# Kernel tuning notes

Measured on AMD Instinct MI355X. Metric: run time of the kernel, lower is better.

The kernel has to match this reference:

```python
import jax, jax.numpy as jnp
import numpy as np

N_NODES = 50000
N_EDGES = 1_600_000
IN_CH, HID_CH, NUM_CLS = 256, 128, 64
THRESHOLD = 0.5  # default forward arg


def setup_inputs() -> dict:
    key = jax.random.key(0)
    k1, k2, k3, k4 = jax.random.split(key, 4)
    x = jax.random.normal(k1, (N_NODES, IN_CH), dtype=jnp.float32)
    edge_index = jax.random.randint(k2, (2, N_EDGES), 0, N_NODES, dtype=jnp.int32)
    W1 = jax.random.normal(k3, (IN_CH, HID_CH), dtype=jnp.float32) * (1.0 / np.sqrt(IN_CH))
    b1 = jnp.zeros((HID_CH,), dtype=jnp.float32)
    W2 = jax.random.normal(k4, (HID_CH, NUM_CLS), dtype=jnp.float32) * (1.0 / np.sqrt(HID_CH))
    b2 = jnp.zeros((NUM_CLS,), dtype=jnp.float32)
    return {"x": x, "edge_index": edge_index, "W1": W1, "b1": b1, "W2": W2, "b2": b2}


def gcn_conv(x, edge_index, W, b):
    """PyG GCNConv: add self-loops, symmetric D^-1/2 (A+I) D^-1/2 normalization,
    linear transform then gather -> weight -> segment-sum scatter, bias after agg."""
    n = x.shape[0]
    loop = jnp.arange(n, dtype=edge_index.dtype)
    src = jnp.concatenate([edge_index[0], loop])  # message source j
    dst = jnp.concatenate([edge_index[1], loop])  # aggregation target i
    deg = jax.ops.segment_sum(jnp.ones_like(src, dtype=x.dtype), dst, num_segments=n)
    dinv = jnp.where(deg > 0, jax.lax.rsqrt(deg), 0.0)
    norm = dinv[src] * dinv[dst]                  # [E+N]
    h = x @ W                                     # [N, out]
    msg = h[src] * norm[:, None]                  # [E+N, out] gather + scale
    agg = jax.ops.segment_sum(msg, dst, num_segments=n)  # scatter-add
    return agg + b


def reference(x, edge_index, W1, b1, W2, b2):
    h = jax.nn.relu(gcn_conv(x, edge_index, W1, b1))
    logits = gcn_conv(h, edge_index, W2, b2)
    probabilities = jax.nn.sigmoid(logits)
    predictions = (probabilities > THRESHOLD).astype(probabilities.dtype)
    return predictions, probabilities
```

## Files before the change

### kernel.cpp

```cpp
#include <hip/hip_runtime.h>
#include <math.h>

#define EPT 16
#define CHUNK (256 * EPT)
#define CAP 12288

typedef __attribute__((ext_vector_type(8))) short s16x8;
typedef __attribute__((ext_vector_type(4))) float f32x4;

__device__ inline unsigned short f2bf(float f) {
    unsigned u = __builtin_bit_cast(unsigned, f);
    u += 0x7fffu + ((u >> 16) & 1u);
    return (unsigned short)(u >> 16);
}
__device__ inline float bf2f(unsigned short h) {
    unsigned u = ((unsigned)h) << 16;
    return __builtin_bit_cast(float, u);
}


__global__ void bucket_scatter_k(const int* __restrict__ src, const int* __restrict__ dst,
                                 int* __restrict__ bfill, unsigned int* __restrict__ bpk,
                                 int E) {
    __shared__ int hist[256], gofs[256], lfill[256];
    int t = threadIdx.x;
    int base = blockIdx.x * CHUNK;
    hist[t] = 0;
    lfill[t] = 0;
    __syncthreads();
    int ds[EPT], ss[EPT];
#pragma unroll
    for (int i = 0; i < EPT; ++i) {
        int e = base + i * 256 + t;
        if (e < E) {
            ds[i] = dst[e];
            ss[i] = src[e];
            atomicAdd(&hist[ds[i] >> 8], 1);
        } else {
            ds[i] = -1;
        }
    }
    __syncthreads();
    if (hist[t]) gofs[t] = atomicAdd(&bfill[t], hist[t]);
    __syncthreads();
#pragma unroll
    for (int i = 0; i < EPT; ++i) {
        if (ds[i] >= 0) {
            int b = ds[i] >> 8;
            int p = atomicAdd(&lfill[b], 1);
            int idx = gofs[b] + p;
            if (idx < CAP)
                bpk[b * CAP + idx] = ((unsigned)(ds[i] & 255) << 16) | (unsigned)ss[i];
        }
    }
}

__global__ void bucket_build_k(const unsigned int* __restrict__ bpk,
                               const int* __restrict__ bfill,
                               unsigned short* __restrict__ csr,
                               int* __restrict__ rbeg, int* __restrict__ rend,
                               float* __restrict__ dinv, int n) {
    __shared__ int hist[256], loff[256], lfill[256], tmp[256];
    __shared__ unsigned short scsr[CAP];
    int b = blockIdx.x, t = threadIdx.x;
    int base = b * CAP;
    int bsize = min(bfill[b], CAP);
    hist[t] = 0;
    lfill[t] = 0;
    __syncthreads();
    for (int idx = t; idx < bsize; idx += 256)
        atomicAdd(&hist[bpk[base + idx] >> 16], 1);
    __syncthreads();
    int deg = hist[t];
    tmp[t] = deg;
    __syncthreads();
    for (int off = 1; off < 256; off <<= 1) {
        int a = (t >= off) ? tmp[t - off] : 0;
        __syncthreads();
        tmp[t] += a;
        __syncthreads();
    }
    loff[t] = tmp[t] - deg;
    int node = (b << 8) + t;
    if (node < n) {
        rbeg[node] = base + loff[t];
        rend[node] = base + loff[t] + deg;
        dinv[node] = rsqrtf((float)(deg + 1));
    }
    __syncthreads();
    for (int idx = t; idx < bsize; idx += 256) {
        unsigned u = bpk[base + idx];
        int ln = (int)(u >> 16);
        int sp = atomicAdd(&lfill[ln], 1);
        scsr[loff[ln] + sp] = (unsigned short)(u & 0xFFFFu);
    }
    __syncthreads();
    for (int idx = t; idx < bsize; idx += 256)
        csr[base + idx] = scsr[idx];
}


__global__ void w1pack_k(const float* __restrict__ W, unsigned short* __restrict__ wh,
                         unsigned short* __restrict__ wl) {
    int e = blockIdx.x * 256 + threadIdx.x;
    int k = e >> 7, col = e & 127;
    float w = W[e];
    unsigned short h = f2bf(w);
    unsigned short l = f2bf(w - bf2f(h));
    int ct = col >> 4, ks = k >> 5;
    int lane = (col & 15) + (((k >> 3) & 3) << 4);
    int i = k & 7;
    size_t idx = ((((size_t)ct * 8 + ks) * 64 + lane) << 3) + i;
    wh[idx] = h;
    wl[idx] = l;
}


__global__ __launch_bounds__(256) void gemm1_k(const float* __restrict__ x,
                                               const unsigned short* __restrict__ wh,
                                               const unsigned short* __restrict__ wl,
                                               const float* __restrict__ dinv,
                                               float* __restrict__ hs, int n) {
    __shared__ __align__(16) unsigned short ah[2 * 8 * 64 * 8];
    __shared__ __align__(16) unsigned short al[2 * 8 * 64 * 8];
    __shared__ __align__(16) unsigned short bh[8 * 64 * 8];
    __shared__ __align__(16) unsigned short bl[8 * 64 * 8];
    int tid = threadIdx.x;
    int wave = tid >> 6, lane = tid & 63;
    int band = wave & 1, cq = wave >> 1;
    int r0 = blockIdx.x * 32;

    for (int v = tid; v < 2048; v += 256) {
        int r = v >> 6;
        int k = (v & 63) << 2;
        int row = r0 + r;
        if (row >= n) row = n - 1;
        float4 xv = *(const float4*)(x + (long long)row * 256 + k);
        int bd = r >> 4, ks = k >> 5;
        int la = (r & 15) + (((k >> 3) & 3) << 4);
        int i0 = k & 7;
        size_t idx = ((((size_t)bd * 8 + ks) * 64 + la) << 3) + i0;
        ushort4 hh, ll;
        hh.x = f2bf(xv.x); ll.x = f2bf(xv.x - bf2f(hh.x));
        hh.y = f2bf(xv.y); ll.y = f2bf(xv.y - bf2f(hh.y));
        hh.z = f2bf(xv.z); ll.z = f2bf(xv.z - bf2f(hh.z));
        hh.w = f2bf(xv.w); ll.w = f2bf(xv.w - bf2f(hh.w));
        *(ushort4*)&ah[idx] = hh;
        *(ushort4*)&al[idx] = ll;
    }

    f32x4 acc[4];
#pragma unroll
    for (int c = 0; c < 4; ++c) acc[c] = (f32x4){0.f, 0.f, 0.f, 0.f};

    const float4* gh = (const float4*)wh;
    const float4* gl = (const float4*)wl;
    for (int ks = 0; ks < 8; ++ks) {
        __syncthreads();
#pragma unroll
        for (int it = 0; it < 2; ++it) {
            int s = it * 256 + tid;
            size_t gi = ((size_t)(s >> 6) * 8 + ks) * 64 + (s & 63);
            ((float4*)bh)[s] = gh[gi];
            ((float4*)bl)[s] = gl[gi];
        }
        __syncthreads();
        size_t aidx = (((size_t)band * 8 + ks) * 64 + lane) << 3;
        s16x8 Ah = *(const s16x8*)&ah[aidx];
        s16x8 Al = *(const s16x8*)&al[aidx];
#pragma unroll
        for (int c = 0; c < 4; ++c) {
            int ct = cq * 4 + c;
            size_t bidx = (((size_t)ct) * 64 + lane) << 3;
            s16x8 Bh = *(const s16x8*)&bh[bidx];
            s16x8 Bl = *(const s16x8*)&bl[bidx];
            acc[c] = __builtin_amdgcn_mfma_f32_16x16x32_bf16(Ah, Bh, acc[c], 0, 0, 0);
            acc[c] = __builtin_amdgcn_mfma_f32_16x16x32_bf16(Ah, Bl, acc[c], 0, 0, 0);
            acc[c] = __builtin_amdgcn_mfma_f32_16x16x32_bf16(Al, Bh, acc[c], 0, 0, 0);
        }
    }

    int colb = cq * 64 + (lane & 15);
    int rbase = r0 + band * 16 + ((lane >> 4) << 2);
#pragma unroll
    for (int reg = 0; reg < 4; ++reg) {
        int row = rbase + reg;
        if (row < n) {
            float di = dinv[row];
#pragma unroll
            for (int c = 0; c < 4; ++c)
                hs[(long long)row * 128 + colb + c * 16] = acc[c][reg] * di;
        }
    }
}


__global__ __launch_bounds__(128) void gemm2_k(const float* __restrict__ h1,
                                               const float* __restrict__ W,
                                               const float* __restrict__ dinv,
                                               float* __restrict__ hs2, int n) {
    __shared__ float xs[32][64];
    int tid = threadIdx.x;
    int cg = tid & 15;
    int rg = tid >> 4;
    int r0 = blockIdx.x * 32;
    float acc[4][4];
#pragma unroll
    for (int r = 0; r < 4; ++r)
#pragma unroll
        for (int c = 0; c < 4; ++c) acc[r][c] = 0.0f;

    for (int kc = 0; kc < 2; ++kc) {
        __syncthreads();
        for (int v = tid; v < 32 * 16; v += 128) {
            int r = v >> 4;
            int k4 = v & 15;
            float4 val = make_float4(0.f, 0.f, 0.f, 0.f);
            int row = r0 + r;
            if (row < n) val = *(const float4*)(h1 + (long long)row * 128 + kc * 64 + k4 * 4);
            *(float4*)&xs[r][k4 * 4] = val;
        }
        __syncthreads();
        const float* Wp = W + (long long)(kc * 64) * 64 + cg * 4;
#pragma unroll 4
        for (int k4 = 0; k4 < 16; ++k4) {
            float4 w0 = *(const float4*)(Wp + (k4 * 4 + 0) * 64);
            float4 w1 = *(const float4*)(Wp + (k4 * 4 + 1) * 64);
            float4 w2 = *(const float4*)(Wp + (k4 * 4 + 2) * 64);
            float4 w3 = *(const float4*)(Wp + (k4 * 4 + 3) * 64);
#pragma unroll
            for (int r = 0; r < 4; ++r) {
                float4 xv = *(const float4*)&xs[rg * 4 + r][k4 * 4];
                acc[r][0] += xv.x * w0.x + xv.y * w1.x + xv.z * w2.x + xv.w * w3.x;
                acc[r][1] += xv.x * w0.y + xv.y * w1.y + xv.z * w2.y + xv.w * w3.y;
                acc[r][2] += xv.x * w0.z + xv.y * w1.z + xv.z * w2.z + xv.w * w3.z;
                acc[r][3] += xv.x * w0.w + xv.y * w1.w + xv.z * w2.w + xv.w * w3.w;
            }
        }
    }
#pragma unroll
    for (int r = 0; r < 4; ++r) {
        int row = r0 + rg * 4 + r;
        if (row < n) {
            float di = dinv[row];
            float4 o = make_float4(acc[r][0] * di, acc[r][1] * di,
                                   acc[r][2] * di, acc[r][3] * di);
            *(float4*)(hs2 + (long long)row * 64 + cg * 4) = o;
        }
    }
}


__global__ void gather1p_k(const float* __restrict__ hs, const int* __restrict__ rbeg,
                           const int* __restrict__ rend, const unsigned short* __restrict__ csr,
                           const float* __restrict__ dinv, const float* __restrict__ b1,
                           float* __restrict__ h1, int n, int gblk) {
    int pass = blockIdx.x / gblk;
    int blk = blockIdx.x - pass * gblk;
    int c0 = pass * 32;
    int g = threadIdx.x >> 3;
    int lane = threadIdx.x & 7;
    int i = blk * 32 + g;
    if (i >= n) return;
    const float* hsc = hs + c0;
    float4 acc = ((const float4*)(hsc + (long long)i * 128))[lane];
    int beg = rbeg[i], end = rend[i];
    int j = beg;
    for (; j + 8 <= end; j += 8) {
        int s0 = csr[j], s1 = csr[j + 1], s2 = csr[j + 2], s3 = csr[j + 3];
        int s4 = csr[j + 4], s5 = csr[j + 5], s6 = csr[j + 6], s7 = csr[j + 7];
        float4 v0 = ((const float4*)(hsc + (long long)s0 * 128))[lane];
        float4 v1 = ((const float4*)(hsc + (long long)s1 * 128))[lane];
        float4 v2 = ((const float4*)(hsc + (long long)s2 * 128))[lane];
        float4 v3 = ((const float4*)(hsc + (long long)s3 * 128))[lane];
        float4 v4 = ((const float4*)(hsc + (long long)s4 * 128))[lane];
        float4 v5 = ((const float4*)(hsc + (long long)s5 * 128))[lane];
        float4 v6 = ((const float4*)(hsc + (long long)s6 * 128))[lane];
        float4 v7 = ((const float4*)(hsc + (long long)s7 * 128))[lane];
        acc.x += (v0.x + v1.x + v2.x + v3.x) + (v4.x + v5.x + v6.x + v7.x);
        acc.y += (v0.y + v1.y + v2.y + v3.y) + (v4.y + v5.y + v6.y + v7.y);
        acc.z += (v0.z + v1.z + v2.z + v3.z) + (v4.z + v5.z + v6.z + v7.z);
        acc.w += (v0.w + v1.w + v2.w + v3.w) + (v4.w + v5.w + v6.w + v7.w);
    }
    for (; j < end; ++j) {
        int s0 = csr[j];
        float4 v0 = ((const float4*)(hsc + (long long)s0 * 128))[lane];
        acc.x += v0.x; acc.y += v0.y; acc.z += v0.z; acc.w += v0.w;
    }
    float di = dinv[i];
    float4 bb = ((const float4*)(b1 + c0))[lane];
    float4 o;
    o.x = fmaxf(di * acc.x + bb.x, 0.0f);
    o.y = fmaxf(di * acc.y + bb.y, 0.0f);
    o.z = fmaxf(di * acc.z + bb.z, 0.0f);
    o.w = fmaxf(di * acc.w + bb.w, 0.0f);
    ((float4*)(h1 + (long long)i * 128 + c0))[lane] = o;
}

__global__ void gather2p_k(const float* __restrict__ hs2, const int* __restrict__ rbeg,
                           const int* __restrict__ rend, const unsigned short* __restrict__ csr,
                           const float* __restrict__ dinv, const float* __restrict__ b2,
                           float* __restrict__ out, int n, int gblk) {
    int pass = blockIdx.x / gblk;
    int blk = blockIdx.x - pass * gblk;
    int c0 = pass * 32;
    int g = threadIdx.x >> 3;
    int lane = threadIdx.x & 7;
    int i = blk * 32 + g;
    if (i >= n) return;
    const float* hc = hs2 + c0;
    float4 acc = ((const float4*)(hc + (long long)i * 64))[lane];
    int beg = rbeg[i], end = rend[i];
    int j = beg;
    for (; j + 8 <= end; j += 8) {
        int s0 = csr[j], s1 = csr[j + 1], s2 = csr[j + 2], s3 = csr[j + 3];
        int s4 = csr[j + 4], s5 = csr[j + 5], s6 = csr[j + 6], s7 = csr[j + 7];
        float4 v0 = ((const float4*)(hc + (long long)s0 * 64))[lane];
        float4 v1 = ((const float4*)(hc + (long long)s1 * 64))[lane];
        float4 v2 = ((const float4*)(hc + (long long)s2 * 64))[lane];
        float4 v3 = ((const float4*)(hc + (long long)s3 * 64))[lane];
        float4 v4 = ((const float4*)(hc + (long long)s4 * 64))[lane];
        float4 v5 = ((const float4*)(hc + (long long)s5 * 64))[lane];
        float4 v6 = ((const float4*)(hc + (long long)s6 * 64))[lane];
        float4 v7 = ((const float4*)(hc + (long long)s7 * 64))[lane];
        acc.x += (v0.x + v1.x + v2.x + v3.x) + (v4.x + v5.x + v6.x + v7.x);
        acc.y += (v0.y + v1.y + v2.y + v3.y) + (v4.y + v5.y + v6.y + v7.y);
        acc.z += (v0.z + v1.z + v2.z + v3.z) + (v4.z + v5.z + v6.z + v7.z);
        acc.w += (v0.w + v1.w + v2.w + v3.w) + (v4.w + v5.w + v6.w + v7.w);
    }
    for (; j < end; ++j) {
        int s0 = csr[j];
        float4 v0 = ((const float4*)(hc + (long long)s0 * 64))[lane];
        acc.x += v0.x; acc.y += v0.y; acc.z += v0.z; acc.w += v0.w;
    }
    float di = dinv[i];
    float4 bb = ((const float4*)(b2 + c0))[lane];
    float lx = di * acc.x + bb.x;
    float ly = di * acc.y + bb.y;
    float lz = di * acc.z + bb.z;
    float lw = di * acc.w + bb.w;
    float4 p;
    p.x = 1.0f / (1.0f + expf(-lx));
    p.y = 1.0f / (1.0f + expf(-ly));
    p.z = 1.0f / (1.0f + expf(-lz));
    p.w = 1.0f / (1.0f + expf(-lw));
    long long total = (long long)n * 64;
    long long o0 = (long long)i * 64 + c0 + lane * 4;
    float4 pr;
    pr.x = (p.x > 0.5f) ? 1.0f : 0.0f;
    pr.y = (p.y > 0.5f) ? 1.0f : 0.0f;
    pr.z = (p.z > 0.5f) ? 1.0f : 0.0f;
    pr.w = (p.w > 0.5f) ? 1.0f : 0.0f;
    *(float4*)(out + o0) = pr;
    *(float4*)(out + total + o0) = p;
}


extern "C" void kernel_launch(void* const* d_in, const int* in_sizes, int n_in,
                              void* d_out, int out_size, void* d_ws, size_t ws_size,
                              hipStream_t stream) {
    const float* x  = (const float*)d_in[0];
    const int*   ei = (const int*)d_in[1];
    const float* W1 = (const float*)d_in[2];
    const float* b1 = (const float*)d_in[3];
    const float* W2 = (const float*)d_in[4];
    const float* b2 = (const float*)d_in[5];
    float* out = (float*)d_out;

    const int n = in_sizes[0] / 256;
    const int E = in_sizes[1] / 2;
    const int* src = ei;
    const int* dst = ei + E;
    const int nb = (n + 255) / 256;

    char* base = (char*)d_ws;
    size_t off = 0;
    auto carve = [&](size_t bytes) -> void* {
        void* p = base + off;
        off = (off + bytes + 255) & ~(size_t)255;
        return p;
    };
    int*   bfill = (int*)  carve(256 * sizeof(int));
    unsigned short* csr = (unsigned short*)carve((size_t)nb * CAP * sizeof(unsigned short));
    int*   rbeg  = (int*)  carve((size_t)n * sizeof(int));
    int*   rend  = (int*)  carve((size_t)n * sizeof(int));
    float* dinv  = (float*)carve((size_t)n * sizeof(float));
    unsigned short* w1h = (unsigned short*)carve(32768 * sizeof(unsigned short));
    unsigned short* w1l = (unsigned short*)carve(32768 * sizeof(unsigned short));
    float* hs0   = (float*)carve((size_t)n * 128 * sizeof(float));
    float* h1    = (float*)carve((size_t)n * 128 * sizeof(float));
    float* hs2   = (float*)carve((size_t)n * 64 * sizeof(float));
    unsigned int* bpk = (unsigned int*)hs0;

    w1pack_k<<<128, 256, 0, stream>>>(W1, w1h, w1l);
    hipMemsetAsync(bfill, 0, 256 * sizeof(int), stream);
    bucket_scatter_k<<<(E + CHUNK - 1) / CHUNK, 256, 0, stream>>>(src, dst, bfill, bpk, E);
    bucket_build_k<<<nb, 256, 0, stream>>>(bpk, bfill, csr, rbeg, rend, dinv, n);

    gemm1_k<<<(n + 31) / 32, 256, 0, stream>>>(x, w1h, w1l, dinv, hs0, n);

    const int gblk = (n + 31) / 32;
    gather1p_k<<<4 * gblk, 256, 0, stream>>>(hs0, rbeg, rend, csr, dinv, b1, h1, n, gblk);

    gemm2_k<<<(n + 31) / 32, 128, 0, stream>>>(h1, W2, dinv, hs2, n);

    gather2p_k<<<2 * gblk, 256, 0, stream>>>(hs2, rbeg, rend, csr, dinv, b2, out, n, gblk);
}
```

Baseline: 230.4 us.

## Sort nodes by degree within buckets for gather balance; fuse W1 pack into prep

bucket_build_k now builds a per-bucket permutation of nodes ordered by clamped degree. Both gather kernels process nodes in that order, so lanes in a wave have similar edge counts and less divergence. W1 bf16 split packing is merged into the bucket scatter kernel as extra blocks, removing one launch. The cost is an extra perm lookup and less contiguous output row writes.

```diff
diff --git a/kernel.cpp b/kernel.cpp
--- a/kernel.cpp
+++ b/kernel.cpp
@@ -19,11 +19,25 @@
 }
 
 
-__global__ void bucket_scatter_k(const int* __restrict__ src, const int* __restrict__ dst,
-                                 int* __restrict__ bfill, unsigned int* __restrict__ bpk,
-                                 int E) {
+__global__ void prep_k(const int* __restrict__ src, const int* __restrict__ dst,
+                       int* __restrict__ bfill, unsigned int* __restrict__ bpk, int E, int SB,
+                       const float* __restrict__ W1,
+                       unsigned short* __restrict__ w1h, unsigned short* __restrict__ w1l) {
     __shared__ int hist[256], gofs[256], lfill[256];
     int t = threadIdx.x;
+    if (blockIdx.x >= SB) {
+        int e = (blockIdx.x - SB) * 256 + t;
+        int k = e >> 7, col = e & 127;
+        float w = W1[e];
+        unsigned short h = f2bf(w), l = f2bf(w - bf2f(h));
+        int ct = col >> 4, ks = k >> 5;
+        int la = (col & 15) + (((k >> 3) & 3) << 4);
+        int i = k & 7;
+        size_t idx = ((((size_t)ct * 8 + ks) * 64 + la) << 3) + i;
+        w1h[idx] = h;
+        w1l[idx] = l;
+        return;
+    }
     int base = blockIdx.x * CHUNK;
     hist[t] = 0;
     lfill[t] = 0;
@@ -55,18 +69,22 @@
     }
 }
 
+
 __global__ void bucket_build_k(const unsigned int* __restrict__ bpk,
                                const int* __restrict__ bfill,
                                unsigned short* __restrict__ csr,
                                int* __restrict__ rbeg, int* __restrict__ rend,
-                               float* __restrict__ dinv, int n) {
+                               float* __restrict__ dinv, unsigned short* __restrict__ perm,
+                               int n) {
     __shared__ int hist[256], loff[256], lfill[256], tmp[256];
+    __shared__ int h2[64];
     __shared__ unsigned short scsr[CAP];
     int b = blockIdx.x, t = threadIdx.x;
     int base = b * CAP;
     int bsize = min(bfill[b], CAP);
     hist[t] = 0;
     lfill[t] = 0;
+    if (t < 64) h2[t] = 0;
     __syncthreads();
     for (int idx = t; idx < bsize; idx += 256)
         atomicAdd(&hist[bpk[base + idx] >> 16], 1);
@@ -82,10 +100,28 @@
     }
     loff[t] = tmp[t] - deg;
     int node = (b << 8) + t;
+    int dc = min(deg, 63);
     if (node < n) {
         rbeg[node] = base + loff[t];
         rend[node] = base + loff[t] + deg;
         dinv[node] = rsqrtf((float)(deg + 1));
+        atomicAdd(&h2[dc], 1);
+    }
+    perm[(b << 8) + t] = 0xFFFFu;
+    __syncthreads();
+    if (t == 0) {
+        int s = 0;
+#pragma unroll
+        for (int i2 = 0; i2 < 64; ++i2) {
+            int v = h2[i2];
+            h2[i2] = s;
+            s += v;
+        }
+    }
+    __syncthreads();
+    if (node < n) {
+        int rank = atomicAdd(&h2[dc], 1);
+        perm[(b << 8) + rank] = (unsigned short)node;
     }
     __syncthreads();
     for (int idx = t; idx < bsize; idx += 256) {
@@ -97,22 +133,6 @@
     __syncthreads();
     for (int idx = t; idx < bsize; idx += 256)
         csr[base + idx] = scsr[idx];
-}
-
-
-__global__ void w1pack_k(const float* __restrict__ W, unsigned short* __restrict__ wh,
-                         unsigned short* __restrict__ wl) {
-    int e = blockIdx.x * 256 + threadIdx.x;
-    int k = e >> 7, col = e & 127;
-    float w = W[e];
-    unsigned short h = f2bf(w);
-    unsigned short l = f2bf(w - bf2f(h));
-    int ct = col >> 4, ks = k >> 5;
-    int lane = (col & 15) + (((k >> 3) & 3) << 4);
-    int i = k & 7;
-    size_t idx = ((((size_t)ct * 8 + ks) * 64 + lane) << 3) + i;
-    wh[idx] = h;
-    wl[idx] = l;
 }
 
 
@@ -253,6 +273,7 @@
 
 __global__ void gather1p_k(const float* __restrict__ hs, const int* __restrict__ rbeg,
                            const int* __restrict__ rend, const unsigned short* __restrict__ csr,
+                           const unsigned short* __restrict__ perm,
                            const float* __restrict__ dinv, const float* __restrict__ b1,
                            float* __restrict__ h1, int n, int gblk) {
     int pass = blockIdx.x / gblk;
@@ -260,7 +281,7 @@
     int c0 = pass * 32;
     int g = threadIdx.x >> 3;
     int lane = threadIdx.x & 7;
-    int i = blk * 32 + g;
+    int i = perm[blk * 32 + g];
     if (i >= n) return;
     const float* hsc = hs + c0;
     float4 acc = ((const float4*)(hsc + (long long)i * 128))[lane];
@@ -299,6 +320,7 @@
 
 __global__ void gather2p_k(const float* __restrict__ hs2, const int* __restrict__ rbeg,
                            const int* __restrict__ rend, const unsigned short* __restrict__ csr,
+                           const unsigned short* __restrict__ perm,
                            const float* __restrict__ dinv, const float* __restrict__ b2,
                            float* __restrict__ out, int n, int gblk) {
     int pass = blockIdx.x / gblk;
@@ -306,7 +328,7 @@
     int c0 = pass * 32;
     int g = threadIdx.x >> 3;
     int lane = threadIdx.x & 7;
-    int i = blk * 32 + g;
+    int i = perm[blk * 32 + g];
     if (i >= n) return;
     const float* hc = hs2 + c0;
     float4 acc = ((const float4*)(hc + (long long)i * 64))[lane];
@@ -385,6 +407,7 @@
     int*   rbeg  = (int*)  carve((size_t)n * sizeof(int));
     int*   rend  = (int*)  carve((size_t)n * sizeof(int));
     float* dinv  = (float*)carve((size_t)n * sizeof(float));
+    unsigned short* perm = (unsigned short*)carve((size_t)nb * 256 * sizeof(unsigned short));
     unsigned short* w1h = (unsigned short*)carve(32768 * sizeof(unsigned short));
     unsigned short* w1l = (unsigned short*)carve(32768 * sizeof(unsigned short));
     float* hs0   = (float*)carve((size_t)n * 128 * sizeof(float));
@@ -392,17 +415,19 @@
     float* hs2   = (float*)carve((size_t)n * 64 * sizeof(float));
     unsigned int* bpk = (unsigned int*)hs0;
 
-    w1pack_k<<<128, 256, 0, stream>>>(W1, w1h, w1l);
+    const int SB = (E + CHUNK - 1) / CHUNK;
+    const int PB = 32768 / 256;
+
     hipMemsetAsync(bfill, 0, 256 * sizeof(int), stream);
-    bucket_scatter_k<<<(E + CHUNK - 1) / CHUNK, 256, 0, stream>>>(src, dst, bfill, bpk, E);
-    bucket_build_k<<<nb, 256, 0, stream>>>(bpk, bfill, csr, rbeg, rend, dinv, n);
+    prep_k<<<SB + PB, 256, 0, stream>>>(src, dst, bfill, bpk, E, SB, W1, w1h, w1l);
+    bucket_build_k<<<nb, 256, 0, stream>>>(bpk, bfill, csr, rbeg, rend, dinv, perm, n);
 
     gemm1_k<<<(n + 31) / 32, 256, 0, stream>>>(x, w1h, w1l, dinv, hs0, n);
 
-    const int gblk = (n + 31) / 32;
-    gather1p_k<<<4 * gblk, 256, 0, stream>>>(hs0, rbeg, rend, csr, dinv, b1, h1, n, gblk);
+    const int gblk = nb * 8;
+    gather1p_k<<<4 * gblk, 256, 0, stream>>>(hs0, rbeg, rend, csr, perm, dinv, b1, h1, n, gblk);
 
     gemm2_k<<<(n + 31) / 32, 128, 0, stream>>>(h1, W2, dinv, hs2, n);
 
-    gather2p_k<<<2 * gblk, 256, 0, stream>>>(hs2, rbeg, rend, csr, dinv, b2, out, n, gblk);
-}
+    gather2p_k<<<2 * gblk, 256, 0, stream>>>(hs2, rbeg, rend, csr, perm, dinv, b2, out, n, gblk);
+}
```

Measured after the change: 262.5 us. 1.14x slower.
